# Optimization experiments

Measured on AMD Instinct MI355X. Metric: run time of the kernel, lower is better.

## Reference

```python
import jax, jax.numpy as jnp
import numpy as np

VOCAB = 100000
DIM = 512
N_POS = 4096
N_NEG = 4096
N_NEU = 2048
CONSISTENCY_WEIGHT = 0.5
SPARSITY_WEIGHT = 0.1


def setup_inputs() -> dict:
    key = jax.random.key(0)
    ks = jax.random.split(key, 7)
    embeddings = jax.random.normal(ks[0], (VOCAB, DIM), dtype=jnp.float32)
    pos_ids = jax.random.randint(ks[1], (N_POS,), 0, VOCAB, dtype=jnp.int64 if jax.config.jax_enable_x64 else jnp.int32)
    pos_dims = jax.random.randint(ks[2], (N_POS,), 0, DIM, dtype=pos_ids.dtype)
    neg_ids = jax.random.randint(ks[3], (N_NEG,), 0, VOCAB, dtype=pos_ids.dtype)
    neg_dims = jax.random.randint(ks[4], (N_NEG,), 0, DIM, dtype=pos_ids.dtype)
    neu_ids = jax.random.randint(ks[5], (N_NEU,), 0, VOCAB, dtype=pos_ids.dtype)
    neu_dims = jax.random.randint(ks[6], (N_NEU,), 0, DIM, dtype=pos_ids.dtype)
    return {"embeddings": embeddings, "pos_ids": pos_ids, "pos_dims": pos_dims,
            "neg_ids": neg_ids, "neg_dims": neg_dims, "neu_ids": neu_ids, "neu_dims": neu_dims}


def _signed_class_loss(embeddings, word_ids, dim_ids, positive: bool):
    # Gather the full embedding rows once; each constraint reads one row.  [N, D]
    vecs = embeddings[word_ids]
    t = jnp.take_along_axis(vecs, dim_ids[:, None], axis=1)[:, 0]  # target-dim values [N]
    abs_t = jnp.abs(t)
    if positive:
        # wrong sign (t<=0): |t|+0.1 penalty; right sign: small reward -0.1*t
        sign_loss = jnp.where(t <= 0, abs_t + 0.1, -t * 0.1)
    else:
        # wrong sign (t>=0): |t|+0.1 penalty; right sign: -0.1*|t| reward
        sign_loss = jnp.where(t >= 0, abs_t + 0.1, -abs_t * 0.1)
    # mean(|vec[other_dims]|) == (sum|vec| - |t|) / (D-1)
    D = embeddings.shape[1]
    sparsity = SPARSITY_WEIGHT * (jnp.sum(jnp.abs(vecs), axis=1) - abs_t) / (D - 1)
    return jnp.sum(sign_loss + sparsity)


def reference(embeddings, pos_ids, pos_dims, neg_ids, neg_dims, neu_ids, neu_dims):
    pos_loss = _signed_class_loss(embeddings, pos_ids, pos_dims, positive=True)
    neg_loss = _signed_class_loss(embeddings, neg_ids, neg_dims, positive=False)
    # neutral: 2*|v[word, dim]|; only the target entry is read
    neu_vals = embeddings[neu_ids, neu_dims]
    neu_loss = jnp.sum(2.0 * jnp.abs(neu_vals))
    num_constraints = pos_ids.shape[0] + neg_ids.shape[0] + neu_ids.shape[0]
    total = pos_loss + neg_loss + neu_loss
    return CONSISTENCY_WEIGHT * (total / num_constraints)
```

## Files before the change

### kernel.cpp

```cpp
#include <hip/hip_runtime.h>


#define DCL_DIM   512
#define DCL_NPOS  4096
#define DCL_NNEG  4096
#define DCL_NNEU  2048
#define DCL_NCON  (DCL_NPOS + DCL_NNEG + DCL_NNEU)
#define DCL_SIGNED_BLOCKS ((DCL_NPOS + DCL_NNEG) / 4)
#define DCL_NEU_BLOCKS    (DCL_NNEU / 256)
#define DCL_GRID  (DCL_SIGNED_BLOCKS + DCL_NEU_BLOCKS)
#define DCL_NPART (DCL_GRID * 4)

__global__ __launch_bounds__(256) void dcl_main(
    const float* __restrict__ emb,
    const int*   __restrict__ pos_ids, const int* __restrict__ pos_dims,
    const int*   __restrict__ neg_ids, const int* __restrict__ neg_dims,
    const int*   __restrict__ neu_ids, const int* __restrict__ neu_dims,
    float* __restrict__ partials)
{
    const int lane = threadIdx.x & 63;
    const int wv   = threadIdx.x >> 6;

    float contrib;

    if (blockIdx.x < DCL_SIGNED_BLOCKS) {
        const int c = blockIdx.x * 4 + wv;
        const bool is_pos = (c < DCL_NPOS);
        int id, dim;
        if (is_pos) { id = pos_ids[c];            dim = pos_dims[c]; }
        else        { id = neg_ids[c - DCL_NPOS]; dim = neg_dims[c - DCL_NPOS]; }

        const float4* r4 = (const float4*)(emb + (size_t)id * DCL_DIM);

        const float4 a = r4[lane];
        const float4 b = r4[lane + 64];

        const int comp = dim & 3;
        const float ca = (comp == 0) ? a.x : (comp == 1) ? a.y : (comp == 2) ? a.z : a.w;
        const float cb = (comp == 0) ? b.x : (comp == 1) ? b.y : (comp == 2) ? b.z : b.w;
        const float cand = (dim < 256) ? ca : cb;
        const float t = __shfl(cand, (dim >> 2) & 63, 64);

        float s = fabsf(a.x) + fabsf(a.y) + fabsf(a.z) + fabsf(a.w)
                + fabsf(b.x) + fabsf(b.y) + fabsf(b.z) + fabsf(b.w);
        #pragma unroll
        for (int o = 32; o >= 1; o >>= 1)
            s += __shfl_down(s, o, 64);

        const float at = fabsf(t);
        float sign_loss;
        if (is_pos) sign_loss = (t <= 0.0f) ? (at + 0.1f) : (-0.1f * t);
        else        sign_loss = (t >= 0.0f) ? (at + 0.1f) : (-0.1f * at);
        contrib = sign_loss + 0.1f * (s - at) * (1.0f / 511.0f);
    } else {
        const int idx = (blockIdx.x - DCL_SIGNED_BLOCKS) * 256 + threadIdx.x;
        const float v = emb[(size_t)neu_ids[idx] * DCL_DIM + neu_dims[idx]];
        float c2 = 2.0f * fabsf(v);
        #pragma unroll
        for (int o = 32; o >= 1; o >>= 1)
            c2 += __shfl_down(c2, o, 64);
        contrib = c2;
    }

    if (lane == 0)
        partials[blockIdx.x * 4 + wv] = contrib;
}

__global__ __launch_bounds__(256) void dcl_reduce(
    const float* __restrict__ partials, float* __restrict__ out)
{
    float s = 0.0f;
    for (int i = threadIdx.x; i < DCL_NPART; i += 256)
        s += partials[i];

    #pragma unroll
    for (int o = 32; o >= 1; o >>= 1)
        s += __shfl_down(s, o, 64);

    __shared__ float sm[4];
    const int lane = threadIdx.x & 63;
    const int wv   = threadIdx.x >> 6;
    if (lane == 0) sm[wv] = s;
    __syncthreads();
    if (threadIdx.x == 0)
        out[0] = (sm[0] + sm[1] + sm[2] + sm[3]) * (0.5f / (float)DCL_NCON);
}

extern "C" void kernel_launch(void* const* d_in, const int* in_sizes, int n_in,
                              void* d_out, int out_size, void* d_ws, size_t ws_size,
                              hipStream_t stream)
{
    const float* emb      = (const float*)d_in[0];
    const int*   pos_ids  = (const int*)d_in[1];
    const int*   pos_dims = (const int*)d_in[2];
    const int*   neg_ids  = (const int*)d_in[3];
    const int*   neg_dims = (const int*)d_in[4];
    const int*   neu_ids  = (const int*)d_in[5];
    const int*   neu_dims = (const int*)d_in[6];

    float* partials = (float*)d_ws;

    dcl_main<<<DCL_GRID, 256, 0, stream>>>(emb, pos_ids, pos_dims,
                                           neg_ids, neg_dims,
                                           neu_ids, neu_dims, partials);
    dcl_reduce<<<1, 256, 0, stream>>>(partials, (float*)d_out);
}
```

Measured before the change: 251.9 us.

## Fuse final reduction into main kernel via last-block atomic counter

Merges the two-kernel structure into one kernel. The last block to finish, found through an atomic counter, reduces the per-block partials and writes the output, so the separate reduce launch goes away. Neutral constraints are folded into the signed-loss blocks, one per block on thread 255, which removes the extra neutral blocks. It adds a memset launch to reset the counter and an atomic per block.

After: 292.2 us. 16.0% more time.

```diff
diff --git a/kernel.cpp b/kernel.cpp
--- a/kernel.cpp
+++ b/kernel.cpp
@@ -6,84 +6,85 @@
 #define DCL_NNEG  4096
 #define DCL_NNEU  2048
 #define DCL_NCON  (DCL_NPOS + DCL_NNEG + DCL_NNEU)
-#define DCL_SIGNED_BLOCKS ((DCL_NPOS + DCL_NNEG) / 4)
-#define DCL_NEU_BLOCKS    (DCL_NNEU / 256)
-#define DCL_GRID  (DCL_SIGNED_BLOCKS + DCL_NEU_BLOCKS)
-#define DCL_NPART (DCL_GRID * 4)
+#define DCL_BLOCKS 2048
 
-__global__ __launch_bounds__(256) void dcl_main(
+__global__ __launch_bounds__(256) void dcl_fused(
     const float* __restrict__ emb,
     const int*   __restrict__ pos_ids, const int* __restrict__ pos_dims,
     const int*   __restrict__ neg_ids, const int* __restrict__ neg_dims,
     const int*   __restrict__ neu_ids, const int* __restrict__ neu_dims,
-    float* __restrict__ partials)
+    float* __restrict__ partials, unsigned int* __restrict__ counter,
+    float* __restrict__ out)
 {
     const int lane = threadIdx.x & 63;
     const int wv   = threadIdx.x >> 6;
 
-    float contrib;
+    __shared__ float sm[5];
+    __shared__ int   last_flag;
+    __shared__ float red[4];
 
-    if (blockIdx.x < DCL_SIGNED_BLOCKS) {
-        const int c = blockIdx.x * 4 + wv;
-        const bool is_pos = (c < DCL_NPOS);
-        int id, dim;
-        if (is_pos) { id = pos_ids[c];            dim = pos_dims[c]; }
-        else        { id = neg_ids[c - DCL_NPOS]; dim = neg_dims[c - DCL_NPOS]; }
-
-        const float4* r4 = (const float4*)(emb + (size_t)id * DCL_DIM);
-
-        const float4 a = r4[lane];
-        const float4 b = r4[lane + 64];
-
-        const int comp = dim & 3;
-        const float ca = (comp == 0) ? a.x : (comp == 1) ? a.y : (comp == 2) ? a.z : a.w;
-        const float cb = (comp == 0) ? b.x : (comp == 1) ? b.y : (comp == 2) ? b.z : b.w;
-        const float cand = (dim < 256) ? ca : cb;
-        const float t = __shfl(cand, (dim >> 2) & 63, 64);
-
-        float s = fabsf(a.x) + fabsf(a.y) + fabsf(a.z) + fabsf(a.w)
-                + fabsf(b.x) + fabsf(b.y) + fabsf(b.z) + fabsf(b.w);
-        #pragma unroll
-        for (int o = 32; o >= 1; o >>= 1)
-            s += __shfl_down(s, o, 64);
-
-        const float at = fabsf(t);
-        float sign_loss;
-        if (is_pos) sign_loss = (t <= 0.0f) ? (at + 0.1f) : (-0.1f * t);
-        else        sign_loss = (t >= 0.0f) ? (at + 0.1f) : (-0.1f * at);
-        contrib = sign_loss + 0.1f * (s - at) * (1.0f / 511.0f);
-    } else {
-        const int idx = (blockIdx.x - DCL_SIGNED_BLOCKS) * 256 + threadIdx.x;
-        const float v = emb[(size_t)neu_ids[idx] * DCL_DIM + neu_dims[idx]];
-        float c2 = 2.0f * fabsf(v);
-        #pragma unroll
-        for (int o = 32; o >= 1; o >>= 1)
-            c2 += __shfl_down(c2, o, 64);
-        contrib = c2;
+    float neu_contrib = 0.0f;
+    if (threadIdx.x == 255) {
+        const int nid  = neu_ids[blockIdx.x];
+        const int ndim = neu_dims[blockIdx.x];
+        neu_contrib = 2.0f * fabsf(emb[(size_t)nid * DCL_DIM + ndim]);
     }
 
-    if (lane == 0)
-        partials[blockIdx.x * 4 + wv] = contrib;
-}
+    const int  c      = blockIdx.x * 4 + wv;
+    const bool is_pos = (c < DCL_NPOS);
+    int id, dim;
+    if (is_pos) { id = pos_ids[c];            dim = pos_dims[c]; }
+    else        { id = neg_ids[c - DCL_NPOS]; dim = neg_dims[c - DCL_NPOS]; }
 
-__global__ __launch_bounds__(256) void dcl_reduce(
-    const float* __restrict__ partials, float* __restrict__ out)
-{
-    float s = 0.0f;
-    for (int i = threadIdx.x; i < DCL_NPART; i += 256)
-        s += partials[i];
+    const float4* r4 = (const float4*)(emb + (size_t)id * DCL_DIM);
+    const float4 a = r4[lane];
+    const float4 b = r4[lane + 64];
 
+    const int comp = dim & 3;
+    const float ca = (comp == 0) ? a.x : (comp == 1) ? a.y : (comp == 2) ? a.z : a.w;
+    const float cb = (comp == 0) ? b.x : (comp == 1) ? b.y : (comp == 2) ? b.z : b.w;
+    const float t  = __shfl((dim < 256) ? ca : cb, (dim >> 2) & 63, 64);
+
+    float s = fabsf(a.x) + fabsf(a.y) + fabsf(a.z) + fabsf(a.w)
+            + fabsf(b.x) + fabsf(b.y) + fabsf(b.z) + fabsf(b.w);
     #pragma unroll
     for (int o = 32; o >= 1; o >>= 1)
         s += __shfl_down(s, o, 64);
 
-    __shared__ float sm[4];
-    const int lane = threadIdx.x & 63;
-    const int wv   = threadIdx.x >> 6;
-    if (lane == 0) sm[wv] = s;
+    const float at = fabsf(t);
+    float sign_loss;
+    if (is_pos) sign_loss = (t <= 0.0f) ? (at + 0.1f) : (-0.1f * t);
+    else        sign_loss = (t >= 0.0f) ? (at + 0.1f) : (-0.1f * at);
+    const float contrib = sign_loss + 0.1f * (s - at) * (1.0f / 511.0f);
+
+    if (lane == 0)          sm[wv] = contrib;
+    if (threadIdx.x == 255) sm[4]  = neu_contrib;
     __syncthreads();
-    if (threadIdx.x == 0)
-        out[0] = (sm[0] + sm[1] + sm[2] + sm[3]) * (0.5f / (float)DCL_NCON);
+
+    if (threadIdx.x == 0) {
+        const float p = sm[0] + sm[1] + sm[2] + sm[3] + sm[4];
+        __hip_atomic_store(&partials[blockIdx.x], p,
+                           __ATOMIC_RELAXED, __HIP_MEMORY_SCOPE_AGENT);
+        const unsigned old = __hip_atomic_fetch_add(counter, 1u,
+                           __ATOMIC_ACQ_REL, __HIP_MEMORY_SCOPE_AGENT);
+        last_flag = (old == DCL_BLOCKS - 1);
+    }
+    __syncthreads();
+
+    if (last_flag) {
+        float fs = 0.0f;
+        #pragma unroll
+        for (int k = 0; k < DCL_BLOCKS / 256; ++k)
+            fs += __hip_atomic_load(&partials[k * 256 + threadIdx.x],
+                                    __ATOMIC_RELAXED, __HIP_MEMORY_SCOPE_AGENT);
+        #pragma unroll
+        for (int o = 32; o >= 1; o >>= 1)
+            fs += __shfl_down(fs, o, 64);
+        if (lane == 0) red[wv] = fs;
+        __syncthreads();
+        if (threadIdx.x == 0)
+            out[0] = (red[0] + red[1] + red[2] + red[3]) * (0.5f / (float)DCL_NCON);
+    }
 }
 
 extern "C" void kernel_launch(void* const* d_in, const int* in_sizes, int n_in,
@@ -98,10 +99,13 @@
     const int*   neu_ids  = (const int*)d_in[5];
     const int*   neu_dims = (const int*)d_in[6];
 
-    float* partials = (float*)d_ws;
+    float*        partials = (float*)d_ws;
+    unsigned int* counter  = (unsigned int*)((char*)d_ws + DCL_BLOCKS * sizeof(float));
 
-    dcl_main<<<DCL_GRID, 256, 0, stream>>>(emb, pos_ids, pos_dims,
-                                           neg_ids, neg_dims,
-                                           neu_ids, neu_dims, partials);
-    dcl_reduce<<<1, 256, 0, stream>>>(partials, (float*)d_out);
+    hipMemsetAsync(counter, 0, sizeof(unsigned int), stream);
+
+    dcl_fused<<<DCL_BLOCKS, 256, 0, stream>>>(emb, pos_ids, pos_dims,
+                                              neg_ids, neg_dims,
+                                              neu_ids, neu_dims,
+                                              partials, counter, (float*)d_out);
 }
```
